# Performance work log

Hardware: AMD Instinct MI355X
Metric: run time of the kernel (lower is better)

Reference implementation:

```python
import jax, jax.numpy as jnp
import numpy as np

L = 2048  # sequence length
V = 2048  # num_tokens == channel width (one-hot embedding)
B = 4     # batch


def _pos_bias(v_table):
    # pos[i,j] = max(i-j, 0); embed via [L,1] table -> [L,L]
    i = jnp.arange(L)
    pos = jnp.maximum(i[:, None] - i[None, :], 0)
    return v_table[pos, 0]


def setup_inputs() -> dict:
    key = jax.random.key(0)
    ks = jax.random.split(key, 11)
    idx = jax.random.randint(ks[0], (B, L), 0, V)
    lin = lambda k, std: (jax.random.normal(k, (V, V), dtype=jnp.float32) * std)
    return {
        "idx": idx,
        # layer_zero: all std=1 (explicit re-init in torch code)
        "Wq0": lin(ks[1], 1.0), "Wk0": lin(ks[2], 1.0), "Wv0": lin(ks[3], 1.0),
        # layer_one: Wk std=1 (re-init), Wv std=0.02 (default init); Wq is zero-fn
        "Wk1": lin(ks[4], 1.0), "Wv1": lin(ks[5], 0.02),
        # layer_two: Wq,Wv std=1 (re-init), Wk std=0.02 (default)
        "Wq2": lin(ks[6], 1.0), "Wk2": lin(ks[7], 0.02), "Wv2": lin(ks[8], 1.0),
        # relative-position embedding tables [L,1], std=0.02
        "v0": jax.random.normal(ks[9], (L, 1), dtype=jnp.float32) * 0.02,
        "v1": jax.random.normal(ks[10], (L, 1), dtype=jnp.float32) * 0.02,
    }


def reference(idx, Wq0, Wk0, Wv0, Wk1, Wv1, Wq2, Wk2, Wv2, v0, v1):
    e = jax.nn.one_hot(idx, V, dtype=jnp.float32)            # [B,L,V]
    tril = jnp.tril(jnp.ones((L, L), dtype=bool))
    p0 = _pos_bias(v0)                                       # [L,L]
    p1 = _pos_bias(v1)

    # layer_zero(e, e): scores = Q@K^T + sum_e(K)[:,None]*pos, tril, @V (no softmax)
    K0 = e @ Wk0.T
    Q0 = e @ Wq0.T
    V0 = e @ Wv0.T
    s0 = jnp.einsum('bqv,bkv->bqk', Q0, K0) + K0.sum(-1)[:, :, None] * p0[None]
    l0 = jnp.where(tril, s0, 0.0) @ V0                       # [B,L,V]

    # layer_one(l0, e): Wq is zero-fn -> only the pos-bias term survives
    K1 = e @ Wk1.T
    V1 = l0 @ Wv1.T
    s1 = K1.sum(-1)[:, :, None] * p1[None]
    l1 = jnp.where(tril, s1, 0.0) @ V1

    # layer_two(e, l1): v is zero-fn -> no pos bias
    K2 = l1 @ Wk2.T
    Q2 = e @ Wq2.T
    V2 = e @ Wv2.T
    s2 = jnp.einsum('bqv,bkv->bqk', Q2, K2)
    logits = jnp.where(tril, s2, 0.0) @ V2                   # [B,L,V]
    return logits
```

## Files before the change

kernel.cpp:

```cpp
#include <hip/hip_runtime.h>

typedef float f32x4 __attribute__((ext_vector_type(4)));
typedef short s16x8 __attribute__((ext_vector_type(8)));

constexpr int L = 2048;
constexpr int V = 2048;
constexpr int NB = 4;
constexpr size_t VV  = (size_t)V * V;
constexpr size_t BLV = (size_t)NB * L * V;
constexpr size_t LV  = (size_t)L * V;

__device__ __forceinline__ unsigned short f2bf(float f) {
    unsigned u = __float_as_uint(f);
    u = (u + 0x7FFFu + ((u >> 16) & 1u)) >> 16;
    return (unsigned short)u;
}
__device__ __forceinline__ float bf2f(unsigned short s) {
    return __uint_as_float(((unsigned)s) << 16);
}

__device__ __forceinline__ void gload16(const unsigned short* g, unsigned short* l) {
    auto gp = (const __attribute__((address_space(1))) unsigned int*)g;
    auto lp = (__attribute__((address_space(3))) unsigned int*)l;
    __builtin_amdgcn_global_load_lds(gp, lp, 16, 0, 0);
}

#define SBAR __builtin_amdgcn_sched_barrier(0)


__device__ __forceinline__ void stage_half(const unsigned short* G, int r0, int k0,
                                           unsigned short* slice, int wave, int lane) {
    int rl = lane >> 2, slot = lane & 3;
    #pragma unroll
    for (int r = 0; r < 2; ++r) {
        int rowl = r * 128 + wave * 16 + rl;
        int colg = k0 + ((slot ^ ((rowl >> 1) & 3)) * 8);
        gload16(G + (size_t)(r0 + rowl) * 2048 + colg,
                slice + (size_t)(r * 128 + wave * 16) * 32);
    }
}

__device__ __forceinline__ s16x8 fragx(const unsigned short* slice, int row, int kc) {
    return *(const s16x8*)&slice[row * 32 + ((kc ^ ((row >> 1) & 3)) * 8)];
}

__device__ __forceinline__ void kloop32(const unsigned short* Ab, const unsigned short* Bb,
                                        int m0, int n0, int kt0, int NT, unsigned short* lds,
                                        int wave, int lane, int wr, int wc,
                                        f32x4 (&acc)[8][4]) {
    const int r15 = lane & 15, kc = lane >> 4;

    stage_half(Ab, m0, kt0 * 32,        lds + 0,     wave, lane);
    stage_half(Bb, n0, kt0 * 32,        lds + 8192,  wave, lane);
    stage_half(Ab, m0, (kt0 + 1) * 32,  lds + 16384, wave, lane);
    stage_half(Bb, n0, (kt0 + 1) * 32,  lds + 24576, wave, lane);
    asm volatile("s_waitcnt vmcnt(4)" ::: "memory");
    __builtin_amdgcn_s_barrier();
    SBAR;

    int cb = 0;
    for (int t = 0; t < NT; ++t) {
        const unsigned short* cur = lds + cb * 16384;
        int sb = cb + 2; if (sb >= 3) sb -= 3;
        unsigned short* stg = lds + sb * 16384;
        const bool pre = (t + 2 < NT);
        const int k2 = (kt0 + t + 2) * 32;

        s16x8 b0[4], a[4], a2[4];
        #pragma unroll
        for (int nf = 0; nf < 4; ++nf)
            b0[nf] = fragx(cur + 8192, wc * 64 + nf * 16 + r15, kc);
        #pragma unroll
        for (int mf = 0; mf < 4; ++mf)
            a[mf] = fragx(cur, wr * 128 + mf * 16 + r15, kc);
        if (pre) stage_half(Ab, m0, k2, stg, wave, lane);
        __builtin_amdgcn_s_setprio(1);
        #pragma unroll
        for (int mf = 0; mf < 4; ++mf)
            #pragma unroll
            for (int nf = 0; nf < 4; ++nf)
                acc[mf][nf] = __builtin_amdgcn_mfma_f32_16x16x32_bf16(a[mf], b0[nf], acc[mf][nf], 0, 0, 0);
        __builtin_amdgcn_s_setprio(0);

        #pragma unroll
        for (int mf = 0; mf < 4; ++mf)
            a2[mf] = fragx(cur, wr * 128 + (mf + 4) * 16 + r15, kc);
        if (pre) stage_half(Bb, n0, k2, stg + 8192, wave, lane);
        __builtin_amdgcn_s_setprio(1);
        #pragma unroll
        for (int mf = 0; mf < 4; ++mf)
            #pragma unroll
            for (int nf = 0; nf < 4; ++nf)
                acc[mf + 4][nf] = __builtin_amdgcn_mfma_f32_16x16x32_bf16(a2[mf], b0[nf], acc[mf + 4][nf], 0, 0, 0);
        __builtin_amdgcn_s_setprio(0);

        if (pre)               { asm volatile("s_waitcnt vmcnt(4)" ::: "memory"); }
        else if (t + 2 == NT)  { asm volatile("s_waitcnt vmcnt(0)" ::: "memory"); }
        __builtin_amdgcn_s_barrier();
        SBAR;
        if (++cb == 3) cb = 0;
    }
}

__device__ __forceinline__ int xcd_swz(int flat, int total) {
    return (flat & 7) * (total >> 3) + (flat >> 3);
}

template<int OUTM, bool TOEP>
__global__ __launch_bounds__(512, 2) void gemm_big(
    const unsigned short* __restrict__ A, size_t sA,
    const unsigned short* __restrict__ B, size_t sB,
    float* __restrict__ outF, unsigned short* __restrict__ outH, size_t sO,
    const int* __restrict__ idxp, const float* __restrict__ ks)
{
    __shared__ __align__(16) unsigned short lds[3 * 16384];

    const int tid  = threadIdx.x;
    const int lane = tid & 63, wave = tid >> 6;
    const int wr = wave >> 2, wc = wave & 3;
    const int r15 = lane & 15, kc = lane >> 4;

    int bx, by, bz, half = 0;
    if constexpr (TOEP) {
        bx = blockIdx.y; by = blockIdx.x;
        bz = blockIdx.z & 3;
        half = blockIdx.z >> 2;
    } else {
        int gx = gridDim.x, gy = gridDim.y;
        int flat = blockIdx.x + gx * (blockIdx.y + gy * blockIdx.z);
        int total = gx * gy * gridDim.z;
        int n2 = xcd_swz(flat, total);
        bx = n2 % gx; n2 /= gx; by = n2 % gy; bz = n2 / gy;
    }
    const int m0 = by * 256, n0 = bx * 256;

    int kt0 = 0, NT;
    if constexpr (TOEP) {
        int NTh = 4 * (bx + 1);
        kt0 = half * NTh;
        NT = NTh;
    } else {
        NT = 64;
    }

    const unsigned short* Ab = A + (size_t)bz * sA;
    const unsigned short* Bb = B + (size_t)bz * sB;

    f32x4 acc[8][4];
    const f32x4 zf = {0.f, 0.f, 0.f, 0.f};
    #pragma unroll
    for (int i = 0; i < 8; ++i)
        #pragma unroll
        for (int j = 0; j < 4; ++j) acc[i][j] = zf;

    kloop32(Ab, Bb, m0, n0, kt0, NT, lds, wave, lane, wr, wc, acc);

    float csc[4];
    if constexpr (TOEP) {
        #pragma unroll
        for (int nf = 0; nf < 4; ++nf) {
            int gcol = n0 + wc * 64 + nf * 16 + r15;
            csc[nf] = ks[idxp[bz * L + gcol]];
        }
    }
    unsigned short* oH = outH;
    if constexpr (TOEP) oH += (size_t)half * BLV;
    #pragma unroll
    for (int mf = 0; mf < 8; ++mf) {
        #pragma unroll
        for (int r = 0; r < 4; ++r) {
            int grow = m0 + wr * 128 + mf * 16 + kc * 4 + r;
            #pragma unroll
            for (int nf = 0; nf < 4; ++nf) {
                float v = acc[mf][nf][r];
                if constexpr (TOEP) v *= csc[nf];
                int gcol = n0 + wc * 64 + nf * 16 + r15;
                size_t o = (size_t)bz * sO + (size_t)grow * 2048 + gcol;
                if constexpr (OUTM == 0) outF[o] = v;
                else                     oH[o] = f2bf(v);
            }
        }
    }
}

struct PDesc { const unsigned short* A; const unsigned short* B; float* oF; unsigned short* oH; };

__global__ __launch_bounds__(512, 2) void gemm_pre_big(PDesc d0, PDesc d1, PDesc d2) {
    __shared__ __align__(16) unsigned short lds[3 * 16384];

    const int tid  = threadIdx.x;
    const int lane = tid & 63, wave = tid >> 6;
    const int wr = wave >> 2, wc = wave & 3;
    const int r15 = lane & 15, kc = lane >> 4;

    int flat = blockIdx.x + 8 * (blockIdx.y + 8 * blockIdx.z);
    int total = 64 * gridDim.z;
    int n2 = xcd_swz(flat, total);
    int bx = n2 & 7; n2 >>= 3;
    int by = n2 & 7; n2 >>= 3;
    PDesc d = (n2 == 0) ? d0 : (n2 == 1) ? d1 : d2;
    const int m0 = by * 256, n0 = bx * 256;

    f32x4 acc[8][4];
    const f32x4 zf = {0.f, 0.f, 0.f, 0.f};
    #pragma unroll
    for (int i = 0; i < 8; ++i)
        #pragma unroll
        for (int j = 0; j < 4; ++j) acc[i][j] = zf;

    kloop32(d.A, d.B, m0, n0, 0, 64, lds, wave, lane, wr, wc, acc);

    const bool isF = (d.oF != nullptr);
    #pragma unroll
    for (int mf = 0; mf < 8; ++mf) {
        #pragma unroll
        for (int r = 0; r < 4; ++r) {
            int grow = m0 + wr * 128 + mf * 16 + kc * 4 + r;
            #pragma unroll
            for (int nf = 0; nf < 4; ++nf) {
                float v = acc[mf][nf][r];
                int gcol = n0 + wc * 64 + nf * 16 + r15;
                size_t o = (size_t)grow * 2048 + gcol;
                if (isF) d.oF[o] = v;
                else     d.oH[o] = f2bf(v);
            }
        }
    }
}

__global__ __launch_bounds__(512, 2) void gemm_preK(const unsigned short* __restrict__ A,
                                                    const unsigned short* __restrict__ B,
                                                    float* __restrict__ outP) {
    __shared__ __align__(16) unsigned short lds[3 * 16384];

    const int tid  = threadIdx.x;
    const int lane = tid & 63, wave = tid >> 6;
    const int wr = wave >> 2, wc = wave & 3;
    const int r15 = lane & 15, kc = lane >> 4;

    int flat = blockIdx.x + 8 * (blockIdx.y + 8 * blockIdx.z);
    int n2 = xcd_swz(flat, 256);
    int bx = n2 & 7; n2 >>= 3;
    int by = n2 & 7; n2 >>= 3;
    int z = n2;
    const int m0 = by * 256, n0 = bx * 256;

    const unsigned short* Ab = A + z * 512;
    const unsigned short* Bb = B + z * 512;
    float* outF = outP + (size_t)z * VV;

    f32x4 acc[8][4];
    const f32x4 zf = {0.f, 0.f, 0.f, 0.f};
    #pragma unroll
    for (int i = 0; i < 8; ++i)
        #pragma unroll
        for (int j = 0; j < 4; ++j) acc[i][j] = zf;

    kloop32(Ab, Bb, m0, n0, 0, 16, lds, wave, lane, wr, wc, acc);

    #pragma unroll
    for (int mf = 0; mf < 8; ++mf) {
        #pragma unroll
        for (int r = 0; r < 4; ++r) {
            int grow = m0 + wr * 128 + mf * 16 + kc * 4 + r;
            #pragma unroll
            for (int nf = 0; nf < 4; ++nf) {
                int gcol = n0 + wc * 64 + nf * 16 + r15;
                outF[(size_t)grow * 2048 + gcol] = acc[mf][nf][r];
            }
        }
    }
}

__global__ __launch_bounds__(256) void reduce4_cast(const float* __restrict__ P,
                                                    unsigned short* __restrict__ H) {
    int i = blockIdx.x * 256 + threadIdx.x;
    const float4* p0 = (const float4*)P;
    const float4* p1 = (const float4*)(P + VV);
    const float4* p2 = (const float4*)(P + 2 * VV);
    const float4* p3 = (const float4*)(P + 3 * VV);
    float4 a = p0[i], b = p1[i], c = p2[i], d = p3[i];
    ushort4 h;
    h.x = f2bf(a.x + b.x + c.x + d.x);
    h.y = f2bf(a.y + b.y + c.y + d.y);
    h.z = f2bf(a.z + b.z + c.z + d.z);
    h.w = f2bf(a.w + b.w + c.w + d.w);
    ((ushort4*)H)[i] = h;
}


__global__ __launch_bounds__(256) void colsum2(const float* __restrict__ W0, float* __restrict__ o0,
                                               const float* __restrict__ W1, float* __restrict__ o1) {
    const float* W = blockIdx.y ? W1 : W0;
    float* out = blockIdx.y ? o1 : o0;
    int r0 = blockIdx.x * 8;
    int c = threadIdx.x;
    float s[8];
    #pragma unroll
    for (int i = 0; i < 8; ++i) s[i] = 0.f;
    for (int r = 0; r < 8; ++r) {
        const float* row = W + (size_t)(r0 + r) * V;
        #pragma unroll
        for (int i = 0; i < 8; ++i) s[i] += row[c + i * 256];
    }
    #pragma unroll
    for (int i = 0; i < 8; ++i) atomicAdd(&out[c + i * 256], s[i]);
}

__global__ void init_kernel(float* __restrict__ ks0, float* __restrict__ ks1) {
    int i = blockIdx.x * 256 + threadIdx.x;
    if (i < 2048) { ks0[i] = 0.f; ks1[i] = 0.f; }
}

__global__ __launch_bounds__(256) void tb_fill(const float* __restrict__ v1,
                                               unsigned short* __restrict__ TBh) {
    int n = blockIdx.x;
    int c0 = threadIdx.x * 8;
    s16x8 hv;
    #pragma unroll
    for (int i = 0; i < 8; ++i) {
        int k = c0 + i;
        float f = (k <= n) ? v1[n - k] : 0.f;
        hv[i] = (short)f2bf(f);
    }
    *(s16x8*)&TBh[(size_t)n * 2048 + c0] = hv;
}

struct TDesc { const float* A; unsigned short* Th; };

__global__ void transpose_cast_multi(TDesc d0, TDesc d1, TDesc d2, TDesc d3, TDesc d4) {
    TDesc d;
    switch (blockIdx.z) {
        case 0: d = d0; break;
        case 1: d = d1; break;
        case 2: d = d2; break;
        case 3: d = d3; break;
        default: d = d4; break;
    }
    __shared__ float tile[32][33];
    int x = blockIdx.x * 32 + threadIdx.x;
    int y0 = blockIdx.y * 32;
    for (int r = threadIdx.y; r < 32; r += 8)
        tile[r][threadIdx.x] = d.A[(size_t)(y0 + r) * V + x];
    __syncthreads();
    int xo = blockIdx.y * 32 + threadIdx.x;
    int yo0 = blockIdx.x * 32;
    for (int r = threadIdx.y; r < 32; r += 8)
        d.Th[(size_t)(yo0 + r) * V + xo] = f2bf(tile[threadIdx.x][r]);
}

__global__ __launch_bounds__(256) void cast2_kernel(const float* __restrict__ A0,
                                                    unsigned short* __restrict__ H0,
                                                    const float* __restrict__ A1,
                                                    unsigned short* __restrict__ H1) {
    const float* A = blockIdx.y ? A1 : A0;
    unsigned short* H = blockIdx.y ? H1 : H0;
    int i = blockIdx.x * 256 + threadIdx.x;
    float4 f = ((const float4*)A)[i];
    ushort4 h;
    h.x = f2bf(f.x); h.y = f2bf(f.y); h.z = f2bf(f.z); h.w = f2bf(f.w);
    ((ushort4*)H)[i] = h;
}


__global__ __launch_bounds__(256) void scatterA_kernel(const int* __restrict__ idx,
                                                       const float* __restrict__ G0,
                                                       const float* __restrict__ ks0,
                                                       const float* __restrict__ v0,
                                                       unsigned short* __restrict__ Th) {
    __shared__ float buck[4 * 2048];
    int tid = threadIdx.x;
    const float4 z4 = make_float4(0.f, 0.f, 0.f, 0.f);
    #pragma unroll
    for (int i = 0; i < 8; ++i) ((float4*)buck)[tid + i * 256] = z4;
    __syncthreads();

    int b = blockIdx.y, q0 = blockIdx.x * 4;
    int qr = tid >> 6, lane = tid & 63;
    int q = q0 + qr;
    const int* idxb = idx + b * L;
    int iq = idxb[q];
    float kq = ks0[iq];
    const float* Grow = G0 + (size_t)iq * V;
    float* brow = buck + qr * 2048;

    int k = lane;
    for (; k + 192 <= q; k += 256) {
        int i0 = idxb[k], i1 = idxb[k + 64], i2 = idxb[k + 128], i3 = idxb[k + 192];
        float g0 = Grow[i0], g1 = Grow[i1], g2 = Grow[i2], g3 = Grow[i3];
        float w0 = v0[q - k], w1 = v0[q - k - 64], w2 = v0[q - k - 128], w3 = v0[q - k - 192];
        atomicAdd(&brow[i0], g0 + kq * w0);
        atomicAdd(&brow[i1], g1 + kq * w1);
        atomicAdd(&brow[i2], g2 + kq * w2);
        atomicAdd(&brow[i3], g3 + kq * w3);
    }
    for (; k <= q; k += 64) {
        int ik = idxb[k];
        atomicAdd(&brow[ik], Grow[ik] + kq * v0[q - k]);
    }
    __syncthreads();
    size_t base = ((size_t)b * L + q0) * V;
    #pragma unroll
    for (int it = 0; it < 4; ++it) {
        int i = tid + it * 256;
        s16x8 hv;
        #pragma unroll
        for (int j = 0; j < 8; ++j) hv[j] = (short)f2bf(buck[i * 8 + j]);
        *(s16x8*)&Th[base + (size_t)i * 8] = hv;
    }
}

__global__ __launch_bounds__(256) void scatterC_kernel(const int* __restrict__ idx,
                                                       const unsigned short* __restrict__ T2a,
                                                       const unsigned short* __restrict__ T2b,
                                                       unsigned short* __restrict__ Th) {
    __shared__ float buck[4 * 2048];
    int tid = threadIdx.x;
    const float4 z4 = make_float4(0.f, 0.f, 0.f, 0.f);
    #pragma unroll
    for (int i = 0; i < 8; ++i) ((float4*)buck)[tid + i * 256] = z4;
    __syncthreads();

    int b = blockIdx.y, q0 = blockIdx.x * 4;
    int qr = tid >> 6, lane = tid & 63;
    int q = q0 + qr;
    const int* idxb = idx + b * L;
    int iq = idxb[q];
    size_t roff = ((size_t)b * V + iq) * L;
    const unsigned short* TrA = T2a + roff;
    const unsigned short* TrB = T2b + roff;
    float* brow = buck + qr * 2048;

    int k = lane;
    for (; k + 192 <= q; k += 256) {
        int i0 = idxb[k], i1 = idxb[k + 64], i2 = idxb[k + 128], i3 = idxb[k + 192];
        float t0 = bf2f(TrA[k]) + bf2f(TrB[k]);
        float t1 = bf2f(TrA[k + 64]) + bf2f(TrB[k + 64]);
        float t2 = bf2f(TrA[k + 128]) + bf2f(TrB[k + 128]);
        float t3 = bf2f(TrA[k + 192]) + bf2f(TrB[k + 192]);
        atomicAdd(&brow[i0], t0);
        atomicAdd(&brow[i1], t1);
        atomicAdd(&brow[i2], t2);
        atomicAdd(&brow[i3], t3);
    }
    for (; k <= q; k += 64)
        atomicAdd(&brow[idxb[k]], bf2f(TrA[k]) + bf2f(TrB[k]));
    __syncthreads();
    size_t base = ((size_t)b * L + q0) * V;
    #pragma unroll
    for (int it = 0; it < 4; ++it) {
        int i = tid + it * 256;
        s16x8 hv;
        #pragma unroll
        for (int j = 0; j < 8; ++j) hv[j] = (short)f2bf(buck[i * 8 + j]);
        *(s16x8*)&Th[base + (size_t)i * 8] = hv;
    }
}


extern "C" void kernel_launch(void* const* d_in, const int* in_sizes, int n_in,
                              void* d_out, int out_size, void* d_ws, size_t ws_size,
                              hipStream_t stream) {
    (void)in_sizes; (void)n_in; (void)out_size; (void)ws_size;
    const int*   idx = (const int*)d_in[0];
    const float* Wq0 = (const float*)d_in[1];
    const float* Wk0 = (const float*)d_in[2];
    const float* Wv0 = (const float*)d_in[3];
    const float* Wk1 = (const float*)d_in[4];
    const float* Wv1 = (const float*)d_in[5];
    const float* Wq2 = (const float*)d_in[6];
    const float* Wk2 = (const float*)d_in[7];
    const float* Wv2 = (const float*)d_in[8];
    const float* v0  = (const float*)d_in[9];
    const float* v1  = (const float*)d_in[10];
    float* out = (float*)d_out;

    char* W = (char*)d_ws;
    const size_t MiB = 1024 * 1024;

    unsigned short* PPT = (unsigned short*)W;
    unsigned short* TAh = (unsigned short*)W;
    unsigned short* T2a = (unsigned short*)W;
    unsigned short* T2b = T2a + BLV;
    float* Rp = (float*)(W + 8 * MiB);
    unsigned short* Y1 = (unsigned short*)(W + 64 * MiB);
    unsigned short* Y2 = (unsigned short*)(W + 72 * MiB);
    unsigned short* Uh  = (unsigned short*)(W + 64 * MiB);
    unsigned short* TCh = Uh;
    float* Gf = (float*)(W + 96 * MiB);
    unsigned short* Y4 = (unsigned short*)(W + 112 * MiB);
    unsigned short* X1 = (unsigned short*)(W + 128 * MiB);
    unsigned short* X2 = (unsigned short*)(W + 136 * MiB);
    unsigned short* X3 = (unsigned short*)(W + 144 * MiB);
    unsigned short* X4 = (unsigned short*)(W + 152 * MiB);
    unsigned short* X5 = (unsigned short*)(W + 160 * MiB);
    unsigned short* TBh = (unsigned short*)(W + 168 * MiB);
    float* ks0 = (float*)(W + 192 * MiB);
    float* ks1 = (float*)(W + 192 * MiB + 16 * 1024);

    dim3 blk(256);

    {
        TDesc t0{Wq0, X1}, t1{Wk0, X2}, t2{Wq2, X3}, t3{Wk2, X4}, t4{Wv0, Y1};
        transpose_cast_multi<<<dim3(64, 64, 5), dim3(32, 8), 0, stream>>>(t0, t1, t2, t3, t4);
    }
    cast2_kernel<<<dim3((int)(VV / 4 / 256), 2), blk, 0, stream>>>(Wv1, Y2, Wv2, X5);
    tb_fill<<<dim3(2048), blk, 0, stream>>>(v1, TBh);
    init_kernel<<<dim3(8), blk, 0, stream>>>(ks0, ks1);
    colsum2<<<dim3(256, 2), blk, 0, stream>>>(Wk0, ks0, Wk1, ks1);

    {
        PDesc dG{X1, X2, Gf, nullptr};
        PDesc dM{X3, X4, nullptr, Y4};
        PDesc dP{Y1, Y2, nullptr, PPT};
        gemm_pre_big<<<dim3(8, 8, 3), dim3(512), 0, stream>>>(dG, dM, dP);
    }
    gemm_preK<<<dim3(8, 8, 4), dim3(512), 0, stream>>>(Y4, PPT, Rp);
    reduce4_cast<<<dim3((int)(VV / 4 / 256)), blk, 0, stream>>>(Rp, X1);

    scatterA_kernel<<<dim3(L / 4, NB), blk, 0, stream>>>(idx, Gf, ks0, v0, TAh);

    gemm_big<1, false><<<dim3(8, 8, NB), dim3(512), 0, stream>>>(
        X1, 0, TAh, LV, nullptr, Uh, LV, nullptr, nullptr);

    gemm_big<1, true><<<dim3(8, 8, 2 * NB), dim3(512), 0, stream>>>(
        Uh, LV, TBh, 0, nullptr, T2a, LV, idx, ks1);

    scatterC_kernel<<<dim3(L / 4, NB), blk, 0, stream>>>(idx, T2a, T2b, TCh);

    gemm_big<0, false><<<dim3(8, 32, 1), dim3(512), 0, stream>>>(
        TCh, 0, X5, 0, out, nullptr, 0, nullptr, nullptr);
}
```

Before: 463.6 us.

## Switch GEMM mainloop to 64-wide K tiles with double-buffered LDS

Replaces the triple-buffered 32-wide K pipeline with a double-buffered 64-wide K pipeline in which each iteration processes two 32-column halves. Extra workgroup barriers are placed between fragment reads and staging writes so the next tile can be loaded into the other buffer. The aim is fewer loop iterations and less per-iteration sync and wait overhead per unit of MFMA work. In exchange it adds several more barriers per iteration, raises LDS use to 128KB per block, which may cut occupancy below the two blocks per CU the launch bounds request, and leaves a shorter prefetch distance.

After: 470.9 us. About the same (+1.6%).

```diff
diff --git a/kernel.cpp b/kernel.cpp
--- a/kernel.cpp
+++ b/kernel.cpp
@@ -44,36 +44,36 @@
     return *(const s16x8*)&slice[row * 32 + ((kc ^ ((row >> 1) & 3)) * 8)];
 }
 
-__device__ __forceinline__ void kloop32(const unsigned short* Ab, const unsigned short* Bb,
+__device__ __forceinline__ void kloop64(const unsigned short* Ab, const unsigned short* Bb,
                                         int m0, int n0, int kt0, int NT, unsigned short* lds,
                                         int wave, int lane, int wr, int wc,
                                         f32x4 (&acc)[8][4]) {
     const int r15 = lane & 15, kc = lane >> 4;
-
-    stage_half(Ab, m0, kt0 * 32,        lds + 0,     wave, lane);
-    stage_half(Bb, n0, kt0 * 32,        lds + 8192,  wave, lane);
-    stage_half(Ab, m0, (kt0 + 1) * 32,  lds + 16384, wave, lane);
-    stage_half(Bb, n0, (kt0 + 1) * 32,  lds + 24576, wave, lane);
+    const int kb0 = kt0 * 64;
+
+    stage_half(Ab, m0, kb0,      lds + 0,     wave, lane);
+    stage_half(Bb, n0, kb0,      lds + 16384, wave, lane);
+    stage_half(Ab, m0, kb0 + 32, lds + 8192,  wave, lane);
+    stage_half(Bb, n0, kb0 + 32, lds + 24576, wave, lane);
     asm volatile("s_waitcnt vmcnt(4)" ::: "memory");
-    __builtin_amdgcn_s_barrier();
-    SBAR;
-
-    int cb = 0;
+    SBAR; __builtin_amdgcn_s_barrier(); SBAR;
+
     for (int t = 0; t < NT; ++t) {
-        const unsigned short* cur = lds + cb * 16384;
-        int sb = cb + 2; if (sb >= 3) sb -= 3;
-        unsigned short* stg = lds + sb * 16384;
-        const bool pre = (t + 2 < NT);
-        const int k2 = (kt0 + t + 2) * 32;
-
-        s16x8 b0[4], a[4], a2[4];
+        unsigned short* cur = lds + (t & 1) * 32768;
+        unsigned short* nxt = lds + ((t + 1) & 1) * 32768;
+        const bool pre = (t + 1 < NT);
+        const int k1 = kb0 + (t + 1) * 64;
+
+        s16x8 b0[4], b1[4], a[4];
+
         #pragma unroll
         for (int nf = 0; nf < 4; ++nf)
-            b0[nf] = fragx(cur + 8192, wc * 64 + nf * 16 + r15, kc);
+            b0[nf] = fragx(cur + 16384, wc * 64 + nf * 16 + r15, kc);
         #pragma unroll
         for (int mf = 0; mf < 4; ++mf)
             a[mf] = fragx(cur, wr * 128 + mf * 16 + r15, kc);
-        if (pre) stage_half(Ab, m0, k2, stg, wave, lane);
+        if (pre) stage_half(Ab, m0, k1, nxt, wave, lane);
+        SBAR; __builtin_amdgcn_s_barrier(); SBAR;
         __builtin_amdgcn_s_setprio(1);
         #pragma unroll
         for (int mf = 0; mf < 4; ++mf)
@@ -81,24 +81,57 @@
             for (int nf = 0; nf < 4; ++nf)
                 acc[mf][nf] = __builtin_amdgcn_mfma_f32_16x16x32_bf16(a[mf], b0[nf], acc[mf][nf], 0, 0, 0);
         __builtin_amdgcn_s_setprio(0);
-
-        #pragma unroll
-        for (int mf = 0; mf < 4; ++mf)
-            a2[mf] = fragx(cur, wr * 128 + (mf + 4) * 16 + r15, kc);
-        if (pre) stage_half(Bb, n0, k2, stg + 8192, wave, lane);
+        SBAR; __builtin_amdgcn_s_barrier(); SBAR;
+
+        #pragma unroll
+        for (int mf = 0; mf < 4; ++mf)
+            a[mf] = fragx(cur, wr * 128 + (mf + 4) * 16 + r15, kc);
+        if (pre) stage_half(Bb, n0, k1, nxt + 16384, wave, lane);
+        SBAR; __builtin_amdgcn_s_barrier(); SBAR;
         __builtin_amdgcn_s_setprio(1);
         #pragma unroll
         for (int mf = 0; mf < 4; ++mf)
             #pragma unroll
             for (int nf = 0; nf < 4; ++nf)
-                acc[mf + 4][nf] = __builtin_amdgcn_mfma_f32_16x16x32_bf16(a2[mf], b0[nf], acc[mf + 4][nf], 0, 0, 0);
+                acc[mf + 4][nf] = __builtin_amdgcn_mfma_f32_16x16x32_bf16(a[mf], b0[nf], acc[mf + 4][nf], 0, 0, 0);
         __builtin_amdgcn_s_setprio(0);
-
-        if (pre)               { asm volatile("s_waitcnt vmcnt(4)" ::: "memory"); }
-        else if (t + 2 == NT)  { asm volatile("s_waitcnt vmcnt(0)" ::: "memory"); }
-        __builtin_amdgcn_s_barrier();
         SBAR;
-        if (++cb == 3) cb = 0;
+        if (pre) { asm volatile("s_waitcnt vmcnt(4)" ::: "memory"); }
+        else     { asm volatile("s_waitcnt vmcnt(0)" ::: "memory"); }
+        SBAR; __builtin_amdgcn_s_barrier(); SBAR;
+
+        #pragma unroll
+        for (int nf = 0; nf < 4; ++nf)
+            b1[nf] = fragx(cur + 24576, wc * 64 + nf * 16 + r15, kc);
+        #pragma unroll
+        for (int mf = 0; mf < 4; ++mf)
+            a[mf] = fragx(cur + 8192, wr * 128 + mf * 16 + r15, kc);
+        if (pre) stage_half(Ab, m0, k1 + 32, nxt + 8192, wave, lane);
+        SBAR; __builtin_amdgcn_s_barrier(); SBAR;
+        __builtin_amdgcn_s_setprio(1);
+        #pragma unroll
+        for (int mf = 0; mf < 4; ++mf)
+            #pragma unroll
+            for (int nf = 0; nf < 4; ++nf)
+                acc[mf][nf] = __builtin_amdgcn_mfma_f32_16x16x32_bf16(a[mf], b1[nf], acc[mf][nf], 0, 0, 0);
+        __builtin_amdgcn_s_setprio(0);
+        SBAR; __builtin_amdgcn_s_barrier(); SBAR;
+
+        #pragma unroll
+        for (int mf = 0; mf < 4; ++mf)
+            a[mf] = fragx(cur + 8192, wr * 128 + (mf + 4) * 16 + r15, kc);
+        if (pre) stage_half(Bb, n0, k1 + 32, nxt + 24576, wave, lane);
+        SBAR; __builtin_amdgcn_s_barrier(); SBAR;
+        __builtin_amdgcn_s_setprio(1);
+        #pragma unroll
+        for (int mf = 0; mf < 4; ++mf)
+            #pragma unroll
+            for (int nf = 0; nf < 4; ++nf)
+                acc[mf + 4][nf] = __builtin_amdgcn_mfma_f32_16x16x32_bf16(a[mf], b1[nf], acc[mf + 4][nf], 0, 0, 0);
+        __builtin_amdgcn_s_setprio(0);
+        SBAR;
+        if (pre) { asm volatile("s_waitcnt vmcnt(4)" ::: "memory"); }
+        SBAR; __builtin_amdgcn_s_barrier(); SBAR;
     }
 }
 
@@ -113,7 +146,7 @@
     float* __restrict__ outF, unsigned short* __restrict__ outH, size_t sO,
     const int* __restrict__ idxp, const float* __restrict__ ks)
 {
-    __shared__ __align__(16) unsigned short lds[3 * 16384];
+    __shared__ __align__(16) unsigned short lds[2 * 32768];
 
     const int tid  = threadIdx.x;
     const int lane = tid & 63, wave = tid >> 6;
@@ -136,11 +169,11 @@
 
     int kt0 = 0, NT;
     if constexpr (TOEP) {
-        int NTh = 4 * (bx + 1);
+        int NTh = 2 * (bx + 1);
         kt0 = half * NTh;
         NT = NTh;
     } else {
-        NT = 64;
+        NT = 32;
     }
 
     const unsigned short* Ab = A + (size_t)bz * sA;
@@ -153,7 +186,7 @@
         #pragma unroll
         for (int j = 0; j < 4; ++j) acc[i][j] = zf;
 
-    kloop32(Ab, Bb, m0, n0, kt0, NT, lds, wave, lane, wr, wc, acc);
+    kloop64(Ab, Bb, m0, n0, kt0, NT, lds, wave, lane, wr, wc, acc);
 
     float csc[4];
     if constexpr (TOEP) {
@@ -186,7 +219,7 @@
 struct PDesc { const unsigned short* A; const unsigned short* B; float* oF; unsigned short* oH; };
 
 __global__ __launch_bounds__(512, 2) void gemm_pre_big(PDesc d0, PDesc d1, PDesc d2) {
-    __shared__ __align__(16) unsigned short lds[3 * 16384];
+    __shared__ __align__(16) unsigned short lds[2 * 32768];
 
     const int tid  = threadIdx.x;
     const int lane = tid & 63, wave = tid >> 6;
@@ -208,7 +241,7 @@
         #pragma unroll
         for (int j = 0; j < 4; ++j) acc[i][j] = zf;
 
-    kloop32(d.A, d.B, m0, n0, 0, 64, lds, wave, lane, wr, wc, acc);
+    kloop64(d.A, d.B, m0, n0, 0, 32, lds, wave, lane, wr, wc, acc);
 
     const bool isF = (d.oF != nullptr);
     #pragma unroll
@@ -231,7 +264,7 @@
 __global__ __launch_bounds__(512, 2) void gemm_preK(const unsigned short* __restrict__ A,
                                                     const unsigned short* __restrict__ B,
                                                     float* __restrict__ outP) {
-    __shared__ __align__(16) unsigned short lds[3 * 16384];
+    __shared__ __align__(16) unsigned short lds[2 * 32768];
 
     const int tid  = threadIdx.x;
     const int lane = tid & 63, wave = tid >> 6;
@@ -245,8 +278,6 @@
     int z = n2;
     const int m0 = by * 256, n0 = bx * 256;
 
-    const unsigned short* Ab = A + z * 512;
-    const unsigned short* Bb = B + z * 512;
     float* outF = outP + (size_t)z * VV;
 
     f32x4 acc[8][4];
@@ -256,7 +287,7 @@
         #pragma unroll
         for (int j = 0; j < 4; ++j) acc[i][j] = zf;
 
-    kloop32(Ab, Bb, m0, n0, 0, 16, lds, wave, lane, wr, wc, acc);
+    kloop64(A, B, m0, n0, z * 8, 8, lds, wave, lane, wr, wc, acc);
 
     #pragma unroll
     for (int mf = 0; mf < 8; ++mf) {
```

## Shrink GEMM block tiles to 128x256 with 4 waves for more blocks

Applied to the files above, without the earlier changes.

Changes every GEMM kernel from a 256x256 tile with 8 waves to a 128x256 tile with 4 waves. Each wave now covers all 128 rows and 64 columns. Staging is split into separate A and B loaders, and the LDS ring buffer shrinks to match. Grids double in the M dimension, giving more blocks and finer load balance, especially for the triangular Toeplitz GEMM. The cost is lower operand reuse per block and more total global and L2 traffic for B tiles.

Measured after the change: 477.0 us. 1.03x slower.

```diff
diff --git a/kernel.cpp b/kernel.cpp
--- a/kernel.cpp
+++ b/kernel.cpp
@@ -28,15 +28,27 @@
 #define SBAR __builtin_amdgcn_sched_barrier(0)
 
 
-__device__ __forceinline__ void stage_half(const unsigned short* G, int r0, int k0,
-                                           unsigned short* slice, int wave, int lane) {
+__device__ __forceinline__ void stage_A(const unsigned short* G, int r0, int k0,
+                                        unsigned short* slice, int wave, int lane) {
     int rl = lane >> 2, slot = lane & 3;
     #pragma unroll
-    for (int r = 0; r < 2; ++r) {
-        int rowl = r * 128 + wave * 16 + rl;
+    for (int h = 0; h < 2; ++h) {
+        int rowl = wave * 32 + h * 16 + rl;
         int colg = k0 + ((slot ^ ((rowl >> 1) & 3)) * 8);
         gload16(G + (size_t)(r0 + rowl) * 2048 + colg,
-                slice + (size_t)(r * 128 + wave * 16) * 32);
+                slice + (size_t)(wave * 32 + h * 16) * 32);
+    }
+}
+
+__device__ __forceinline__ void stage_B(const unsigned short* G, int r0, int k0,
+                                        unsigned short* slice, int wave, int lane) {
+    int rl = lane >> 2, slot = lane & 3;
+    #pragma unroll
+    for (int h = 0; h < 4; ++h) {
+        int rowl = wave * 64 + h * 16 + rl;
+        int colg = k0 + ((slot ^ ((rowl >> 1) & 3)) * 8);
+        gload16(G + (size_t)(r0 + rowl) * 2048 + colg,
+                slice + (size_t)(wave * 64 + h * 16) * 32);
     }
 }
 
@@ -46,34 +58,34 @@
 
 __device__ __forceinline__ void kloop32(const unsigned short* Ab, const unsigned short* Bb,
                                         int m0, int n0, int kt0, int NT, unsigned short* lds,
-                                        int wave, int lane, int wr, int wc,
+                                        int wave, int lane, int wc,
                                         f32x4 (&acc)[8][4]) {
     const int r15 = lane & 15, kc = lane >> 4;
 
-    stage_half(Ab, m0, kt0 * 32,        lds + 0,     wave, lane);
-    stage_half(Bb, n0, kt0 * 32,        lds + 8192,  wave, lane);
-    stage_half(Ab, m0, (kt0 + 1) * 32,  lds + 16384, wave, lane);
-    stage_half(Bb, n0, (kt0 + 1) * 32,  lds + 24576, wave, lane);
-    asm volatile("s_waitcnt vmcnt(4)" ::: "memory");
+    stage_A(Ab, m0, kt0 * 32,       lds + 0,             wave, lane);
+    stage_B(Bb, n0, kt0 * 32,       lds + 4096,          wave, lane);
+    stage_A(Ab, m0, (kt0 + 1) * 32, lds + 12288,         wave, lane);
+    stage_B(Bb, n0, (kt0 + 1) * 32, lds + 12288 + 4096,  wave, lane);
+    asm volatile("s_waitcnt vmcnt(6)" ::: "memory");
     __builtin_amdgcn_s_barrier();
     SBAR;
 
     int cb = 0;
     for (int t = 0; t < NT; ++t) {
-        const unsigned short* cur = lds + cb * 16384;
+        const unsigned short* cur = lds + cb * 12288;
         int sb = cb + 2; if (sb >= 3) sb -= 3;
-        unsigned short* stg = lds + sb * 16384;
+        unsigned short* stg = lds + sb * 12288;
         const bool pre = (t + 2 < NT);
         const int k2 = (kt0 + t + 2) * 32;
 
         s16x8 b0[4], a[4], a2[4];
         #pragma unroll
         for (int nf = 0; nf < 4; ++nf)
-            b0[nf] = fragx(cur + 8192, wc * 64 + nf * 16 + r15, kc);
+            b0[nf] = fragx(cur + 4096, wc * 64 + nf * 16 + r15, kc);
         #pragma unroll
         for (int mf = 0; mf < 4; ++mf)
-            a[mf] = fragx(cur, wr * 128 + mf * 16 + r15, kc);
-        if (pre) stage_half(Ab, m0, k2, stg, wave, lane);
+            a[mf] = fragx(cur, mf * 16 + r15, kc);
+        if (pre) stage_A(Ab, m0, k2, stg, wave, lane);
         __builtin_amdgcn_s_setprio(1);
         #pragma unroll
         for (int mf = 0; mf < 4; ++mf)
@@ -84,8 +96,8 @@
 
         #pragma unroll
         for (int mf = 0; mf < 4; ++mf)
-            a2[mf] = fragx(cur, wr * 128 + (mf + 4) * 16 + r15, kc);
-        if (pre) stage_half(Bb, n0, k2, stg + 8192, wave, lane);
+            a2[mf] = fragx(cur, (mf + 4) * 16 + r15, kc);
+        if (pre) stage_B(Bb, n0, k2, stg + 4096, wave, lane);
         __builtin_amdgcn_s_setprio(1);
         #pragma unroll
         for (int mf = 0; mf < 4; ++mf)
@@ -94,7 +106,7 @@
                 acc[mf + 4][nf] = __builtin_amdgcn_mfma_f32_16x16x32_bf16(a2[mf], b0[nf], acc[mf + 4][nf], 0, 0, 0);
         __builtin_amdgcn_s_setprio(0);
 
-        if (pre)               { asm volatile("s_waitcnt vmcnt(4)" ::: "memory"); }
+        if (pre)               { asm volatile("s_waitcnt vmcnt(6)" ::: "memory"); }
         else if (t + 2 == NT)  { asm volatile("s_waitcnt vmcnt(0)" ::: "memory"); }
         __builtin_amdgcn_s_barrier();
         SBAR;
@@ -107,22 +119,23 @@
 }
 
 template<int OUTM, bool TOEP>
-__global__ __launch_bounds__(512, 2) void gemm_big(
+__global__ __launch_bounds__(256, 2) void gemm_big(
     const unsigned short* __restrict__ A, size_t sA,
     const unsigned short* __restrict__ B, size_t sB,
     float* __restrict__ outF, unsigned short* __restrict__ outH, size_t sO,
     const int* __restrict__ idxp, const float* __restrict__ ks)
 {
-    __shared__ __align__(16) unsigned short lds[3 * 16384];
+    __shared__ __align__(16) unsigned short lds[3 * 12288];
 
     const int tid  = threadIdx.x;
     const int lane = tid & 63, wave = tid >> 6;
-    const int wr = wave >> 2, wc = wave & 3;
+    const int wc = wave;
     const int r15 = lane & 15, kc = lane >> 4;
 
     int bx, by, bz, half = 0;
     if constexpr (TOEP) {
-        bx = blockIdx.y; by = blockIdx.x;
+        by = blockIdx.x;
+        bx = blockIdx.y;
         bz = blockIdx.z & 3;
         half = blockIdx.z >> 2;
     } else {
@@ -132,7 +145,7 @@
         int n2 = xcd_swz(flat, total);
         bx = n2 % gx; n2 /= gx; by = n2 % gy; bz = n2 / gy;
     }
-    const int m0 = by * 256, n0 = bx * 256;
+    const int m0 = by * 128, n0 = bx * 256;
 
     int kt0 = 0, NT;
     if constexpr (TOEP) {
@@ -153,7 +166,7 @@
         #pragma unroll
         for (int j = 0; j < 4; ++j) acc[i][j] = zf;
 
-    kloop32(Ab, Bb, m0, n0, kt0, NT, lds, wave, lane, wr, wc, acc);
+    kloop32(Ab, Bb, m0, n0, kt0, NT, lds, wave, lane, wc, acc);
 
     float csc[4];
     if constexpr (TOEP) {
@@ -169,7 +182,7 @@
     for (int mf = 0; mf < 8; ++mf) {
         #pragma unroll
         for (int r = 0; r < 4; ++r) {
-            int grow = m0 + wr * 128 + mf * 16 + kc * 4 + r;
+            int grow = m0 + mf * 16 + kc * 4 + r;
             #pragma unroll
             for (int nf = 0; nf < 4; ++nf) {
                 float v = acc[mf][nf][r];
@@ -185,21 +198,21 @@
 
 struct PDesc { const unsigned short* A; const unsigned short* B; float* oF; unsigned short* oH; };
 
-__global__ __launch_bounds__(512, 2) void gemm_pre_big(PDesc d0, PDesc d1, PDesc d2) {
-    __shared__ __align__(16) unsigned short lds[3 * 16384];
+__global__ __launch_bounds__(256, 2) void gemm_pre_big(PDesc d0, PDesc d1, PDesc d2) {
+    __shared__ __align__(16) unsigned short lds[3 * 12288];
 
     const int tid  = threadIdx.x;
     const int lane = tid & 63, wave = tid >> 6;
-    const int wr = wave >> 2, wc = wave & 3;
+    const int wc = wave;
     const int r15 = lane & 15, kc = lane >> 4;
 
-    int flat = blockIdx.x + 8 * (blockIdx.y + 8 * blockIdx.z);
-    int total = 64 * gridDim.z;
+    int flat = blockIdx.x + 8 * (blockIdx.y + 16 * blockIdx.z);
+    int total = 128 * gridDim.z;
     int n2 = xcd_swz(flat, total);
     int bx = n2 & 7; n2 >>= 3;
-    int by = n2 & 7; n2 >>= 3;
+    int by = n2 & 15; n2 >>= 4;
     PDesc d = (n2 == 0) ? d0 : (n2 == 1) ? d1 : d2;
-    const int m0 = by * 256, n0 = bx * 256;
+    const int m0 = by * 128, n0 = bx * 256;
 
     f32x4 acc[8][4];
     const f32x4 zf = {0.f, 0.f, 0.f, 0.f};
@@ -208,14 +221,14 @@
         #pragma unroll
         for (int j = 0; j < 4; ++j) acc[i][j] = zf;
 
-    kloop32(d.A, d.B, m0, n0, 0, 64, lds, wave, lane, wr, wc, acc);
+    kloop32(d.A, d.B, m0, n0, 0, 64, lds, wave, lane, wc, acc);
 
     const bool isF = (d.oF != nullptr);
     #pragma unroll
     for (int mf = 0; mf < 8; ++mf) {
         #pragma unroll
         for (int r = 0; r < 4; ++r) {
-            int grow = m0 + wr * 128 + mf * 16 + kc * 4 + r;
+            int grow = m0 + mf * 16 + kc * 4 + r;
             #pragma unroll
             for (int nf = 0; nf < 4; ++nf) {
                 float v = acc[mf][nf][r];
@@ -228,25 +241,23 @@
     }
 }
 
-__global__ __launch_bounds__(512, 2) void gemm_preK(const unsigned short* __restrict__ A,
+__global__ __launch_bounds__(256, 2) void gemm_preK(const unsigned short* __restrict__ A,
                                                     const unsigned short* __restrict__ B,
                                                     float* __restrict__ outP) {
-    __shared__ __align__(16) unsigned short lds[3 * 16384];
+    __shared__ __align__(16) unsigned short lds[3 * 12288];
 
     const int tid  = threadIdx.x;
     const int lane = tid & 63, wave = tid >> 6;
-    const int wr = wave >> 2, wc = wave & 3;
+    const int wc = wave;
     const int r15 = lane & 15, kc = lane >> 4;
 
-    int flat = blockIdx.x + 8 * (blockIdx.y + 8 * blockIdx.z);
-    int n2 = xcd_swz(flat, 256);
+    int flat = blockIdx.x + 8 * (blockIdx.y + 16 * blockIdx.z);
+    int n2 = xcd_swz(flat, 512);
     int bx = n2 & 7; n2 >>= 3;
-    int by = n2 & 7; n2 >>= 3;
+    int by = n2 & 15; n2 >>= 4;
     int z = n2;
-    const int m0 = by * 256, n0 = bx * 256;
-
-    const unsigned short* Ab = A + z * 512;
-    const unsigned short* Bb = B + z * 512;
+    const int m0 = by * 128, n0 = bx * 256;
+
     float* outF = outP + (size_t)z * VV;
 
     f32x4 acc[8][4];
@@ -256,13 +267,13 @@
         #pragma unroll
         for (int j = 0; j < 4; ++j) acc[i][j] = zf;
 
-    kloop32(Ab, Bb, m0, n0, 0, 16, lds, wave, lane, wr, wc, acc);
+    kloop32(A, B, m0, n0, z * 16, 16, lds, wave, lane, wc, acc);
 
     #pragma unroll
     for (int mf = 0; mf < 8; ++mf) {
         #pragma unroll
         for (int r = 0; r < 4; ++r) {
-            int grow = m0 + wr * 128 + mf * 16 + kc * 4 + r;
+            int grow = m0 + mf * 16 + kc * 4 + r;
             #pragma unroll
             for (int nf = 0; nf < 4; ++nf) {
                 int gcol = n0 + wc * 64 + nf * 16 + r15;
@@ -513,21 +524,21 @@
         PDesc dG{X1, X2, Gf, nullptr};
         PDesc dM{X3, X4, nullptr, Y4};
         PDesc dP{Y1, Y2, nullptr, PPT};
-        gemm_pre_big<<<dim3(8, 8, 3), dim3(512), 0, stream>>>(dG, dM, dP);
-    }
-    gemm_preK<<<dim3(8, 8, 4), dim3(512), 0, stream>>>(Y4, PPT, Rp);
+        gemm_pre_big<<<dim3(8, 16, 3), blk, 0, stream>>>(dG, dM, dP);
+    }
+    gemm_preK<<<dim3(8, 16, 4), blk, 0, stream>>>(Y4, PPT, Rp);
     reduce4_cast<<<dim3((int)(VV / 4 / 256)), blk, 0, stream>>>(Rp, X1);
 
     scatterA_kernel<<<dim3(L / 4, NB), blk, 0, stream>>>(idx, Gf, ks0, v0, TAh);
 
-    gemm_big<1, false><<<dim3(8, 8, NB), dim3(512), 0, stream>>>(
+    gemm_big<1, false><<<dim3(8, 16, NB), blk, 0, stream>>>(
         X1, 0, TAh, LV, nullptr, Uh, LV, nullptr, nullptr);
 
-    gemm_big<1, true><<<dim3(8, 8, 2 * NB), dim3(512), 0, stream>>>(
+    gemm_big<1, true><<<dim3(16, 8, 2 * NB), blk, 0, stream>>>(
         Uh, LV, TBh, 0, nullptr, T2a, LV, idx, ks1);
 
     scatterC_kernel<<<dim3(L / 4, NB), blk, 0, stream>>>(idx, T2a, T2b, TCh);
 
-    gemm_big<0, false><<<dim3(8, 32, 1), dim3(512), 0, stream>>>(
+    gemm_big<0, false><<<dim3(8, 64, 1), blk, 0, stream>>>(
         TCh, 0, X5, 0, out, nullptr, 0, nullptr, nullptr);
 }
```
